# Performance work log

Measured on AMD Instinct MI355X. Metric: run time of the kernel, lower is better.

Reference implementation:

```python
import jax, jax.numpy as jnp
import numpy as np

B, L, D, H = 4, 2048, 1024, 16
HD = D // H

def setup_inputs() -> dict:
    key = jax.random.key(0)
    ks = jax.random.split(key, 5)
    s = 1.0 / np.sqrt(D)
    return {
        "x": jax.random.normal(ks[0], (B, L, D), dtype=jnp.float32),
        "W_qkv": jax.random.normal(ks[1], (D, 3 * D), dtype=jnp.float32) * s,
        "b_qkv": jnp.zeros((3 * D,), dtype=jnp.float32),
        "W_proj": jax.random.normal(ks[2], (D, D), dtype=jnp.float32) * s,
        "b_proj": jnp.zeros((D,), dtype=jnp.float32),
    }

def reference(x, W_qkv, b_qkv, W_proj, b_proj):
    Bx, Lx, Dx = x.shape
    qkv = x @ W_qkv + b_qkv                      # [B,L,3D]
    q, k, v = jnp.split(qkv, 3, axis=-1)
    # [B,L,D] -> [B,H,L,hd]
    def heads(t):
        return t.reshape(Bx, Lx, H, HD).transpose(0, 2, 1, 3)
    q, k, v = heads(q), heads(k), heads(v)
    scale = 1.0 / np.sqrt(HD)
    scores = jnp.einsum('bhqd,bhkd->bhqk', q, k) * scale   # [B,H,L,L]
    causal = jnp.tril(jnp.ones((Lx, Lx), dtype=bool))
    scores = jnp.where(causal[None, None], scores, -jnp.inf)
    probs = jax.nn.softmax(scores, axis=-1)
    y = jnp.einsum('bhqk,bhkd->bhqd', probs, v)             # [B,H,L,hd]
    y = y.transpose(0, 2, 1, 3).reshape(Bx, Lx, Dx)
    return y @ W_proj + b_proj
```

## Files before the change

kernel.cpp:

```cpp
#include <hip/hip_runtime.h>
#include <stdint.h>

#define DEV __device__ __forceinline__

typedef uint32_t u32;
typedef uint16_t u16;
typedef __attribute__((ext_vector_type(4))) float f32x4;
typedef __attribute__((ext_vector_type(8))) __bf16 bf16x8;

DEV u16 f32_to_bf16(float f) {
  u32 u = __builtin_bit_cast(u32, f);
  u += 0x7FFFu + ((u >> 16) & 1u);
  return (u16)(u >> 16);
}
DEV float bf16_to_f32(u16 h) {
  u32 u = ((u32)h) << 16;
  return __builtin_bit_cast(float, u);
}
DEV bf16x8 load_frag16(const u16* p) {
  return __builtin_bit_cast(bf16x8, *(const uint4*)p);
}
DEV float exp2_fast(float x) {
#if __has_builtin(__builtin_amdgcn_exp2f)
  return __builtin_amdgcn_exp2f(x);
#else
  float r;
  asm("v_exp_f32 %0, %1\n\ts_nop 0" : "=v"(r) : "v"(x));
  return r;
#endif
}
DEV u32 cvt_pk_bf16(float lo, float hi) {
  u32 r;
  asm("v_cvt_pk_bf16_f32 %0, %1, %2" : "=v"(r) : "v"(lo), "v"(hi));
  return r;
}

DEV void gl_lds16(const u16* g, u16* l) {
  __builtin_amdgcn_global_load_lds(
      (__attribute__((address_space(1))) void*)(u16*)g,
      (__attribute__((address_space(3))) void*)l, 16, 0, 0);
}

DEV const u16* swz(const u16* basep, int row, int colByte) {
  return (const u16*)((const char*)basep + row * 128 + (colByte ^ ((row & 7) << 4)));
}
DEV u16* swzw(u16* basep, int row, int colByte) {
  return (u16*)((char*)basep + row * 128 + (colByte ^ ((row & 7) << 4)));
}

__global__ void cvt_f32_bf16(const float* __restrict__ in, u16* __restrict__ out, int n) {
  int i = (blockIdx.x * 256 + threadIdx.x) * 4;
  if (i >= n) return;
  float4 v = *(const float4*)(in + i);
  ushort4 o;
  o.x = f32_to_bf16(v.x); o.y = f32_to_bf16(v.y);
  o.z = f32_to_bf16(v.z); o.w = f32_to_bf16(v.w);
  *(ushort4*)(out + i) = o;
}

__global__ void transpose_cvt(const float* __restrict__ in, u16* __restrict__ out, int R, int C) {
  __shared__ float tile[32][33];
  int bx = blockIdx.x * 32;
  int by = blockIdx.y * 32;
  int tx = threadIdx.x & 31;
  int ty = threadIdx.x >> 5;
#pragma unroll
  for (int i = 0; i < 32; i += 8)
    tile[ty + i][tx] = in[(size_t)(by + ty + i) * C + bx + tx];
  __syncthreads();
#pragma unroll
  for (int i = 0; i < 32; i += 8)
    out[(size_t)(bx + ty + i) * R + by + tx] = f32_to_bf16(tile[tx][ty + i]);
}

__global__ void transpose_v(const u16* __restrict__ qkvb, u16* __restrict__ vTg) {
  const int LDT = 72;
  __shared__ __attribute__((aligned(16))) u16 t[64 * 72];
  int bh = blockIdx.y;
  int b = bh >> 4, h = bh & 15;
  int l0 = blockIdx.x * 64;
  int tid = threadIdx.x;
#pragma unroll
  for (int p = 0; p < 2; ++p) {
    int chunk = p * 256 + tid;
    int row = chunk >> 3, cc = chunk & 7;
    *(uint4*)(t + row * LDT + cc * 8) =
        *(const uint4*)(qkvb + (size_t)(b * 2048 + l0 + row) * 3072 + 2048 + h * 64 + cc * 8);
  }
  __syncthreads();
#pragma unroll
  for (int p = 0; p < 2; ++p) {
    int chunk = p * 256 + tid;
    int d = chunk >> 3, cc = chunk & 7;
    ushort4 o0, o1;
    o0.x = t[(cc * 8 + 0) * LDT + d]; o0.y = t[(cc * 8 + 1) * LDT + d];
    o0.z = t[(cc * 8 + 2) * LDT + d]; o0.w = t[(cc * 8 + 3) * LDT + d];
    o1.x = t[(cc * 8 + 4) * LDT + d]; o1.y = t[(cc * 8 + 5) * LDT + d];
    o1.z = t[(cc * 8 + 6) * LDT + d]; o1.w = t[(cc * 8 + 7) * LDT + d];
    u16* op = vTg + ((size_t)bh * 64 + d) * 2048 + l0;
    *(ushort4*)(op + cc * 8 + 0) = o0;
    *(ushort4*)(op + cc * 8 + 4) = o1;
  }
}

template <int OUT_BF16>
__global__ __launch_bounds__(256, 2) void gemm_bf16(
    const u16* __restrict__ A, const u16* __restrict__ Bt,
    const float* __restrict__ bias, void* __restrict__ Cout,
    int M, int N, int K) {
  __shared__ __attribute__((aligned(16))) u16 As[128 * 64];
  __shared__ __attribute__((aligned(16))) u16 Bs[128 * 64];
  int tid = threadIdx.x;
  u32 nwg = gridDim.x * gridDim.y;
  u32 orig = blockIdx.y * gridDim.x + blockIdx.x;
  u32 wg = (orig & 7) * (nwg >> 3) + (orig >> 3);
  int m0 = (wg / gridDim.x) * 128;
  int n0 = (wg % gridDim.x) * 128;
  int w = tid >> 6, l = tid & 63;
  int wr = w >> 1, wc = w & 1;
  int lr = l & 15, lg = l >> 4;
  int rloc = l >> 3, cc = l & 7;
  int scc8 = (cc ^ rloc) * 8;

  f32x4 acc[4][4];
#pragma unroll
  for (int i = 0; i < 4; i++)
#pragma unroll
    for (int j = 0; j < 4; j++) acc[i][j] = (f32x4)0.0f;

  for (int kt = 0; kt < K; kt += 64) {
    __syncthreads();
#pragma unroll
    for (int qq = 0; qq < 4; ++qq) {
      int row = 32 * w + 8 * qq + rloc;
      gl_lds16(A + (size_t)(m0 + row) * K + kt + scc8, &As[(32 * w + 8 * qq) * 64]);
      gl_lds16(Bt + (size_t)(n0 + row) * K + kt + scc8, &Bs[(32 * w + 8 * qq) * 64]);
    }
    __syncthreads();
#pragma unroll
    for (int kk = 0; kk < 2; ++kk) {
      bf16x8 af[4], bfr[4];
#pragma unroll
      for (int i = 0; i < 4; i++)
        af[i] = load_frag16(swz(As, wr * 64 + i * 16 + lr, kk * 64 + lg * 16));
#pragma unroll
      for (int j = 0; j < 4; j++)
        bfr[j] = load_frag16(swz(Bs, wc * 64 + j * 16 + lr, kk * 64 + lg * 16));
#pragma unroll
      for (int i = 0; i < 4; i++)
#pragma unroll
        for (int j = 0; j < 4; j++)
          acc[i][j] = __builtin_amdgcn_mfma_f32_16x16x32_bf16(af[i], bfr[j], acc[i][j], 0, 0, 0);
    }
  }
#pragma unroll
  for (int i = 0; i < 4; i++) {
#pragma unroll
    for (int j = 0; j < 4; j++) {
      int col = n0 + wc * 64 + j * 16 + lr;
      float bv = bias[col];
#pragma unroll
      for (int r = 0; r < 4; r++) {
        int row = m0 + wr * 64 + i * 16 + lg * 4 + r;
        float v = acc[i][j][r] + bv;
        if (OUT_BF16)
          ((u16*)Cout)[(size_t)row * N + col] = f32_to_bf16(v);
        else
          ((float*)Cout)[(size_t)row * N + col] = v;
      }
    }
  }
}

__global__ __launch_bounds__(256, 2) void attn_kernel(
    const u16* __restrict__ qkvb, const u16* __restrict__ vTg,
    u16* __restrict__ attnb) {
  __shared__ __attribute__((aligned(16))) u16 Ks[2][2 * 64 * 64];
  __shared__ __attribute__((aligned(16))) u16 Vt[2][2 * 64 * 64];
  __shared__ __attribute__((aligned(16))) u16 Pl[4][32 * 64];
  int tid = threadIdx.x;
  int w = tid >> 6, l = tid & 63;
  int lr = l & 15, lg = l >> 4;
  int rloc = l >> 3, cc = l & 7;
  int scc8 = (cc ^ rloc) * 8;
  u32 orig = blockIdx.y * 8 + blockIdx.x;
  u32 wg = (orig & 7) * 64 + (orig >> 3);
  int bx = wg & 7;
  int bh = wg >> 3;
  int b = bh >> 4, h = bh & 15;
  const u16* base = qkvb + (size_t)b * 2048 * 3072;
  const u16* kglob = base + 1024 + h * 64;
  const u16* vbase = vTg + (size_t)bh * 64 * 2048;
  u16* PlW = Pl[w];
  int usub = w >> 1, wl = w & 1;
  const float SCALE = 0.18033688011112042f;

#define STAGE128(bi, tt)                                                        \
  do {                                                                          \
    int kv0_ = (tt) * 128;                                                      \
    _Pragma("unroll")                                                           \
    for (int qq = 0; qq < 4; ++qq) {                                            \
      int lrow_ = 32 * wl + 8 * qq;            \
      gl_lds16(kglob + (size_t)(kv0_ + usub * 64 + lrow_ + rloc) * 3072 + scc8, \
               &Ks[bi][usub * 4096 + lrow_ * 64]);                              \
      gl_lds16(vbase + (size_t)(lrow_ + rloc) * 2048 + kv0_ + usub * 64 + scc8, \
               &Vt[bi][usub * 4096 + lrow_ * 64]);                              \
    }                                                                           \
  } while (0)

  for (int half = 0; half < 2; ++half) {
    int s = half ? 15 - bx : bx;
    int qb = s * 128;
    int nst = s + 1;
    int tmax64 = 2 * s + (w >> 1);

    bf16x8 qf[2][2];
#pragma unroll
    for (int i = 0; i < 2; i++)
#pragma unroll
      for (int kk = 0; kk < 2; kk++) {
        int row = qb + w * 32 + i * 16 + lr;
        uint4 v = *(const uint4*)(base + (size_t)row * 3072 + h * 64 + kk * 32 + lg * 8);
        u32 wd[4] = {v.x, v.y, v.z, v.w};
#pragma unroll
        for (int e = 0; e < 4; e++) {
          float flo = bf16_to_f32((u16)(wd[e] & 0xFFFFu)) * SCALE;
          float fhi = bf16_to_f32((u16)(wd[e] >> 16)) * SCALE;
          wd[e] = cvt_pk_bf16(flo, fhi);
        }
        uint4 sv; sv.x = wd[0]; sv.y = wd[1]; sv.z = wd[2]; sv.w = wd[3];
        qf[i][kk] = __builtin_bit_cast(bf16x8, sv);
      }

    float m_st[2] = {-1e30f, -1e30f};
    float l_st[2] = {0.f, 0.f};
    f32x4 of[2][4];
#pragma unroll
    for (int i = 0; i < 2; i++)
#pragma unroll
      for (int j = 0; j < 4; j++) of[i][j] = (f32x4)0.0f;

    STAGE128(0, 0);

    for (int t = 0; t < nst; ++t) {
      int cur = t & 1;
      __syncthreads();
      if (t + 1 < nst) STAGE128(cur ^ 1, t + 1);

#pragma unroll
      for (int u = 0; u < 2; ++u) {
        int t64 = 2 * t + u;
        if (t64 <= tmax64) {
          const u16* Kb = Ks[cur] + u * 4096;
          const u16* Vb = Vt[cur] + u * 4096;

          f32x4 St[4][2];
#pragma unroll
          for (int j = 0; j < 4; j++)
#pragma unroll
            for (int i = 0; i < 2; i++) St[j][i] = (f32x4)0.0f;
          __builtin_amdgcn_s_setprio(1);
#pragma unroll
          for (int kk = 0; kk < 2; ++kk) {
            bf16x8 kbf[4];
#pragma unroll
            for (int j = 0; j < 4; j++)
              kbf[j] = load_frag16(swz(Kb, j * 16 + lr, kk * 64 + lg * 16));
#pragma unroll
            for (int j = 0; j < 4; j++)
#pragma unroll
              for (int i = 0; i < 2; i++)
                St[j][i] = __builtin_amdgcn_mfma_f32_16x16x32_bf16(kbf[j], qf[i][kk], St[j][i], 0, 0, 0);
          }
          __builtin_amdgcn_s_setprio(0);

          if (t64 == tmax64) {
#pragma unroll
            for (int j = 0; j < 4; j++)
#pragma unroll
              for (int i = 0; i < 2; i++)
#pragma unroll
                for (int r = 0; r < 4; r++) {
                  int kabs = t64 * 64 + j * 16 + lg * 4 + r;
                  int qabs = qb + w * 32 + i * 16 + lr;
                  if (kabs > qabs) St[j][i][r] = -1e30f;
                }
          }

#pragma unroll
          for (int i = 0; i < 2; ++i) {
            float tm = -1e30f;
#pragma unroll
            for (int j = 0; j < 4; j++)
#pragma unroll
              for (int r = 0; r < 4; r++) tm = fmaxf(tm, St[j][i][r]);
            tm = fmaxf(tm, __shfl_xor(tm, 16));
            tm = fmaxf(tm, __shfl_xor(tm, 32));
            if (!__all((int)(tm <= m_st[i] + 10.0f))) {
              float mn = fmaxf(m_st[i], tm);
              float fsc = exp2_fast(m_st[i] - mn);
              m_st[i] = mn;
              l_st[i] *= fsc;
#pragma unroll
              for (int r = 0; r < 4; ++r) {
                float ff = __shfl(fsc, lg * 4 + r);
#pragma unroll
                for (int jd = 0; jd < 4; jd++) of[i][jd][r] *= ff;
              }
            }
            float rs = 0.f;
#pragma unroll
            for (int j = 0; j < 4; ++j) {
              float p0 = exp2_fast(St[j][i][0] - m_st[i]);
              float p1 = exp2_fast(St[j][i][1] - m_st[i]);
              float p2 = exp2_fast(St[j][i][2] - m_st[i]);
              float p3 = exp2_fast(St[j][i][3] - m_st[i]);
              rs += (p0 + p1) + (p2 + p3);
              uint2 pk;
              pk.x = cvt_pk_bf16(p0, p1);
              pk.y = cvt_pk_bf16(p2, p3);
              *(uint2*)swzw(PlW, i * 16 + lr, j * 32 + lg * 8) = pk;
            }
            rs += __shfl_xor(rs, 16);
            rs += __shfl_xor(rs, 32);
            l_st[i] += rs;
          }

          __builtin_amdgcn_s_setprio(1);
#pragma unroll
          for (int ks = 0; ks < 2; ++ks) {
            bf16x8 ap[2], vbf[4];
#pragma unroll
            for (int i = 0; i < 2; i++)
              ap[i] = load_frag16(swz(PlW, i * 16 + lr, ks * 64 + lg * 16));
#pragma unroll
            for (int jd = 0; jd < 4; jd++)
              vbf[jd] = load_frag16(swz(Vb, jd * 16 + lr, ks * 64 + lg * 16));
#pragma unroll
            for (int i = 0; i < 2; i++)
#pragma unroll
              for (int jd = 0; jd < 4; jd++)
                of[i][jd] = __builtin_amdgcn_mfma_f32_16x16x32_bf16(ap[i], vbf[jd], of[i][jd], 0, 0, 0);
          }
          __builtin_amdgcn_s_setprio(0);
        }
      }
    }
    __syncthreads();

#pragma unroll
    for (int i = 0; i < 2; i++) {
#pragma unroll
      for (int r = 0; r < 4; r++) {
        float ls = __shfl(l_st[i], lg * 4 + r);
        float inv = 1.0f / ls;
#pragma unroll
        for (int jd = 0; jd < 4; jd++) {
          int row = qb + w * 32 + i * 16 + lg * 4 + r;
          int col = h * 64 + jd * 16 + lr;
          attnb[((size_t)b * 2048 + row) * 1024 + col] = f32_to_bf16(of[i][jd][r] * inv);
        }
      }
    }
  }
#undef STAGE128
}

extern "C" void kernel_launch(void* const* d_in, const int* in_sizes, int n_in,
                              void* d_out, int out_size, void* d_ws, size_t ws_size,
                              hipStream_t stream) {
  const float* x = (const float*)d_in[0];
  const float* Wqkv = (const float*)d_in[1];
  const float* bqkv = (const float*)d_in[2];
  const float* Wproj = (const float*)d_in[3];
  const float* bproj = (const float*)d_in[4];
  float* out = (float*)d_out;

  char* ws = (char*)d_ws;
  u16* xb    = (u16*)(ws);
  u16* vTg   = (u16*)(ws);
  u16* wqT   = (u16*)(ws + 16777216);
  u16* wpT   = (u16*)(ws + 23068672);
  u16* qkvb  = (u16*)(ws + 25165824);
  u16* attnb = (u16*)(ws + 75497472);

  cvt_f32_bf16<<<8192, 256, 0, stream>>>(x, xb, 8388608);
  transpose_cvt<<<dim3(96, 32), 256, 0, stream>>>(Wqkv, wqT, 1024, 3072);
  transpose_cvt<<<dim3(32, 32), 256, 0, stream>>>(Wproj, wpT, 1024, 1024);
  gemm_bf16<1><<<dim3(24, 64), 256, 0, stream>>>(xb, wqT, bqkv, (void*)qkvb, 8192, 3072, 1024);
  transpose_v<<<dim3(32, 64), 256, 0, stream>>>(qkvb, vTg);
  attn_kernel<<<dim3(8, 64), 256, 0, stream>>>(qkvb, vTg, attnb);
  gemm_bf16<0><<<dim3(8, 64), 256, 0, stream>>>(attnb, wpT, bproj, (void*)out, 8192, 1024, 1024);
}
```

Baseline: 165.1 us.

## Use 256x256-tile 8-wave pipelined GEMM for the QKV projection

```diff
diff --git a/kernel.cpp b/kernel.cpp
--- a/kernel.cpp
+++ b/kernel.cpp
@@ -167,6 +167,156 @@
           ((u16*)Cout)[(size_t)row * N + col] = f32_to_bf16(v);
         else
           ((float*)Cout)[(size_t)row * N + col] = v;
+      }
+    }
+  }
+}
+
+__global__ __launch_bounds__(512, 2) void gemm_bf16_256(
+    const u16* __restrict__ A, const u16* __restrict__ Bt,
+    const float* __restrict__ bias, u16* __restrict__ Cout,
+    int M, int N, int K) {
+  __shared__ __attribute__((aligned(16))) u16 As[2][2][128 * 64];
+  __shared__ __attribute__((aligned(16))) u16 Bs[2][2][128 * 64];
+  int tid = threadIdx.x;
+  int wid = tid >> 6, l = tid & 63;
+  int wm = wid >> 2, wn = wid & 3;
+  int lr = l & 15, lg = l >> 4;
+  int rloc = l >> 3, cc = l & 7;
+  int scc8 = (cc ^ rloc) * 8;
+  u32 nwg = gridDim.x * gridDim.y;
+  u32 orig = blockIdx.y * gridDim.x + blockIdx.x;
+  u32 wg = (orig & 7) * (nwg >> 3) + (orig >> 3);
+  int m0 = (int)(wg / gridDim.x) * 256;
+  int n0 = (int)(wg % gridDim.x) * 256;
+  int nt = K >> 6;
+
+  f32x4 acc[8][4];
+#pragma unroll
+  for (int i = 0; i < 8; i++)
+#pragma unroll
+    for (int j = 0; j < 4; j++) acc[i][j] = (f32x4)0.0f;
+
+#define STA(buf, h, s2)                                                        \
+  do {                                                                         \
+    _Pragma("unroll")                                                          \
+    for (int q = 0; q < 2; ++q) {                                              \
+      int rl_ = wid * 16 + q * 8;                                              \
+      gl_lds16(A + (size_t)(m0 + (h)*128 + rl_ + rloc) * K + (s2)*64 + scc8,   \
+               &As[buf][h][rl_ * 64]);                                         \
+    }                                                                          \
+  } while (0)
+#define STB(buf, h, s2)                                                        \
+  do {                                                                         \
+    _Pragma("unroll")                                                          \
+    for (int q = 0; q < 2; ++q) {                                              \
+      int rl_ = wid * 16 + q * 8;                                              \
+      gl_lds16(Bt + (size_t)(n0 + (h)*128 + rl_ + rloc) * K + (s2)*64 + scc8,  \
+               &Bs[buf][h][rl_ * 64]);                                         \
+    }                                                                          \
+  } while (0)
+
+  STA(0, 0, 0); STA(0, 1, 0); STB(0, 0, 0); STB(0, 1, 0);
+  STB(1, 0, 1); STB(1, 1, 1); STA(1, 0, 1);
+  asm volatile("s_waitcnt vmcnt(6)" ::: "memory");
+  __builtin_amdgcn_s_barrier();
+
+  bf16x8 af[4][2], bf[4][2];
+  int bofs = (wn & 1) * 64;
+
+  for (int s = 0; s < nt; ++s) {
+    int p = s & 1;
+    const u16* Aw = &As[p][wm][0];
+    const u16* Bw = &Bs[p][wn >> 1][0];
+
+#pragma unroll
+    for (int i = 0; i < 4; i++)
+#pragma unroll
+      for (int kk = 0; kk < 2; kk++)
+        af[i][kk] = load_frag16(swz(Aw, i * 16 + lr, kk * 64 + lg * 16));
+#pragma unroll
+    for (int j = 0; j < 2; j++)
+#pragma unroll
+      for (int kk = 0; kk < 2; kk++)
+        bf[j][kk] = load_frag16(swz(Bw, bofs + j * 16 + lr, kk * 64 + lg * 16));
+    if (s + 1 < nt) STA(p ^ 1, 1, s + 1);
+    __builtin_amdgcn_s_barrier();
+    __builtin_amdgcn_s_setprio(1);
+#pragma unroll
+    for (int i = 0; i < 4; i++)
+#pragma unroll
+      for (int j = 0; j < 2; j++)
+#pragma unroll
+        for (int kk = 0; kk < 2; kk++)
+          acc[i][j] = __builtin_amdgcn_mfma_f32_16x16x32_bf16(af[i][kk], bf[j][kk], acc[i][j], 0, 0, 0);
+    __builtin_amdgcn_s_setprio(0);
+    __builtin_amdgcn_s_barrier();
+
+#pragma unroll
+    for (int j = 2; j < 4; j++)
+#pragma unroll
+      for (int kk = 0; kk < 2; kk++)
+        bf[j][kk] = load_frag16(swz(Bw, bofs + j * 16 + lr, kk * 64 + lg * 16));
+    __builtin_amdgcn_s_barrier();
+    __builtin_amdgcn_s_setprio(1);
+#pragma unroll
+    for (int i = 0; i < 4; i++)
+#pragma unroll
+      for (int j = 2; j < 4; j++)
+#pragma unroll
+        for (int kk = 0; kk < 2; kk++)
+          acc[i][j] = __builtin_amdgcn_mfma_f32_16x16x32_bf16(af[i][kk], bf[j][kk], acc[i][j], 0, 0, 0);
+    __builtin_amdgcn_s_setprio(0);
+    __builtin_amdgcn_s_barrier();
+
+#pragma unroll
+    for (int i = 0; i < 4; i++)
+#pragma unroll
+      for (int kk = 0; kk < 2; kk++)
+        af[i][kk] = load_frag16(swz(Aw, 64 + i * 16 + lr, kk * 64 + lg * 16));
+    if (s + 2 < nt) STB(p, 0, s + 2);
+    __builtin_amdgcn_s_barrier();
+    __builtin_amdgcn_s_setprio(1);
+#pragma unroll
+    for (int i = 0; i < 4; i++)
+#pragma unroll
+      for (int j = 0; j < 2; j++)
+#pragma unroll
+        for (int kk = 0; kk < 2; kk++)
+          acc[4 + i][j] = __builtin_amdgcn_mfma_f32_16x16x32_bf16(af[i][kk], bf[j][kk], acc[4 + i][j], 0, 0, 0);
+    __builtin_amdgcn_s_setprio(0);
+    __builtin_amdgcn_s_barrier();
+
+    if (s + 2 < nt) { STB(p, 1, s + 2); STA(p, 0, s + 2); }
+    __builtin_amdgcn_s_barrier();
+    __builtin_amdgcn_s_setprio(1);
+#pragma unroll
+    for (int i = 0; i < 4; i++)
+#pragma unroll
+      for (int j = 2; j < 4; j++)
+#pragma unroll
+        for (int kk = 0; kk < 2; kk++)
+          acc[4 + i][j] = __builtin_amdgcn_mfma_f32_16x16x32_bf16(af[i][kk], bf[j][kk], acc[4 + i][j], 0, 0, 0);
+    __builtin_amdgcn_s_setprio(0);
+    if (s + 2 < nt)
+      asm volatile("s_waitcnt vmcnt(6)" ::: "memory");
+    else
+      asm volatile("s_waitcnt vmcnt(0)" ::: "memory");
+    __builtin_amdgcn_s_barrier();
+  }
+#undef STA
+#undef STB
+
+#pragma unroll
+  for (int i = 0; i < 8; i++) {
+#pragma unroll
+    for (int j = 0; j < 4; j++) {
+      int col = n0 + wn * 64 + j * 16 + lr;
+      float bv = bias[col];
+#pragma unroll
+      for (int r = 0; r < 4; r++) {
+        int row = m0 + wm * 128 + i * 16 + lg * 4 + r;
+        Cout[(size_t)row * N + col] = f32_to_bf16(acc[i][j][r] + bv);
       }
     }
   }
@@ -200,7 +350,7 @@
     int kv0_ = (tt) * 128;                                                      \
     _Pragma("unroll")                                                           \
     for (int qq = 0; qq < 4; ++qq) {                                            \
-      int lrow_ = 32 * wl + 8 * qq;            \
+      int lrow_ = 32 * wl + 8 * qq;                                             \
       gl_lds16(kglob + (size_t)(kv0_ + usub * 64 + lrow_ + rloc) * 3072 + scc8, \
                &Ks[bi][usub * 4096 + lrow_ * 64]);                              \
       gl_lds16(vbase + (size_t)(lrow_ + rloc) * 2048 + kv0_ + usub * 64 + scc8, \
@@ -387,7 +537,7 @@
   cvt_f32_bf16<<<8192, 256, 0, stream>>>(x, xb, 8388608);
   transpose_cvt<<<dim3(96, 32), 256, 0, stream>>>(Wqkv, wqT, 1024, 3072);
   transpose_cvt<<<dim3(32, 32), 256, 0, stream>>>(Wproj, wpT, 1024, 1024);
-  gemm_bf16<1><<<dim3(24, 64), 256, 0, stream>>>(xb, wqT, bqkv, (void*)qkvb, 8192, 3072, 1024);
+  gemm_bf16_256<<<dim3(12, 32), 512, 0, stream>>>(xb, wqT, bqkv, qkvb, 8192, 3072, 1024);
   transpose_v<<<dim3(32, 64), 256, 0, stream>>>(qkvb, vTg);
   attn_kernel<<<dim3(8, 64), 256, 0, stream>>>(qkvb, vTg, attnb);
   gemm_bf16<0><<<dim3(8, 64), 256, 0, stream>>>(attnb, wpT, bproj, (void*)out, 8192, 1024, 1024);
```

Result: slower. 179.0 us (+8.4%).
